# Performance work log

Measured on AMD Instinct MI355X. Metric: run time of the kernel, lower is better.

Reference implementation:

```python
import jax, jax.numpy as jnp
import numpy as np


def setup_inputs() -> dict:
    key = jax.random.key(0)
    ks = jax.random.split(key, 8)
    B, N, C = 4, 2048, 1024
    H, hd, lr, R = 16, 64, 20, 200  # R = low_rank * rank_multi
    s = lambda k, shape, fan: jax.random.normal(k, shape, jnp.float32) / np.sqrt(fan)
    return {
        'x': jax.random.normal(ks[0], (B, N, C), jnp.float32),
        'qk_w': s(ks[1], (2 * C, C), C),
        'proj_w': s(ks[2], (C, C), C),
        'proj_b': jnp.zeros((C,), jnp.float32),
        'we': s(ks[3], (H, R, lr), R),
        'wr': s(ks[4], (H, R, lr), R),
        'cw_w': s(ks[5], (hd, 2 * lr), 2 * lr),
        'cw_b': jnp.zeros((hd,), jnp.float32),
    }


def _l2norm(v, eps=1e-12):
    # matches F.normalize(p=2, dim=-1): x / max(||x||, eps)
    n = jnp.sqrt(jnp.sum(v * v, axis=-1, keepdims=True))
    return v / jnp.maximum(n, eps)


def reference(x, qk_w, proj_w, proj_b, we, wr, cw_w, cw_b):
    B, N, C = x.shape
    H, R, lr = we.shape  # heads, subsample len, low_rank
    hd = C // H
    # qk projection -> q,k: [B,H,N,hd]
    qk = (x @ qk_w.T).reshape(B, N, 2, H, hd).transpose(2, 0, 3, 1, 4)
    q, k = qk[0], qk[1]
    # gen_weights: subsample N positions (embed_len > low_rank*rank_multi branch)
    idx = np.linspace(0, N - 1, R).astype(np.int64)  # static, trunc like torch
    xh = x.transpose(0, 2, 1).reshape(B, H, hd, N)[:, :, :, idx]  # [B,H,hd,R]
    we_b = jnp.einsum('bhdr,hre->bhde', xh, we)  # [B,H,hd,lr]
    wr_b = jnp.einsum('bhdr,hre->bhde', xh, wr)
    # feature map + low-rank scores
    q = _l2norm(q)
    k = _l2norm(k)
    escore = jnp.einsum('bhnd,bhde->bhne', q, we_b)  # [B,H,N,lr]
    rscore = jnp.einsum('bhnd,bhde->bhne', k, wr_b)
    score = jnp.concatenate([escore, rscore], axis=-1)  # [B,H,N,2lr]
    attn = score @ cw_w.T + cw_b  # [B,H,N,hd]
    attn = attn.transpose(0, 2, 1, 3).reshape(B, N, C)
    out = attn @ proj_w.T + proj_b  # dropout is identity at eval
    return out
```

## Files before the change

### kernel.cpp

```cpp
#include <hip/hip_runtime.h>
#include <hip/hip_bf16.h>

constexpr int B_  = 4;
constexpr int N_  = 2048;
constexpr int C_  = 1024;
constexpr int H_  = 16;
constexpr int HD  = 64;
constexpr int LR  = 20;
constexpr int RS  = 200;
constexpr int RP  = 224;
constexpr int RPAD = 232;

typedef __attribute__((ext_vector_type(8))) short bf16x8;
typedef __attribute__((ext_vector_type(4))) float f32x4;

__device__ __forceinline__ float b2f_raw(unsigned short u) {
    union { unsigned int i; float f; } v;
    v.i = ((unsigned int)u) << 16;
    return v.f;
}
__device__ __forceinline__ unsigned short f2b(float f) {
    __hip_bfloat16 h = __float2bfloat16(f);
    return *(unsigned short*)&h;
}
template <bool BF>
__device__ __forceinline__ float ldg(const void* p, size_t i) {
    if constexpr (BF) return b2f_raw(((const unsigned short*)p)[i]);
    else              return ((const float*)p)[i];
}

__device__ __forceinline__ void async_load16(const unsigned short* g, unsigned short* l) {
    __builtin_amdgcn_global_load_lds(
        (const __attribute__((address_space(1))) unsigned int*)(const void*)g,
        (__attribute__((address_space(3))) unsigned int*)(void*)l,
        16, 0, 0);
}

__device__ __forceinline__ bool detect_bf16(const unsigned int* __restrict__ x) {
    const int lane = threadIdx.x & 63;
    int cnt = 0;
    #pragma unroll
    for (int i = 0; i < 16; ++i) {
        const unsigned int w = x[lane * 16 + i];
        const unsigned int e = (w >> 7) & 0xFFu;
        cnt += (e >= 103u && e <= 140u) ? 1 : 0;
    }
    #pragma unroll
    for (int s = 1; s < 64; s <<= 1) cnt += __shfl_xor(cnt, s, 64);
    return cnt > 512;
}

struct CvtArgs {
    const void* src[5];
    unsigned short* dst[5];
    int size[5];
};

template <bool BF>
__device__ void gwc_body(const void* __restrict__ x_raw,
                         const void* __restrict__ we_raw,
                         const void* __restrict__ wr_raw,
                         const void* __restrict__ cw_raw,
                         unsigned short* __restrict__ we2t,
                         unsigned short* __restrict__ wr2t,
                         unsigned short* __restrict__ sx,
                         unsigned short* __restrict__ sx2,
                         unsigned short* __restrict__ wl,
                         float* __restrict__ cwl,
                         int blk) {
    const int bh    = blk >> 2;
    const int dhalf = (blk >> 1) & 1;
    const int qk    = blk & 1;
    const int b = bh >> 4;
    const int h = bh & 15;
    const int t    = threadIdx.x;
    const int wave = t >> 6;
    const int lane = t & 63;

    {
        const int dout = t >> 2;
        const int e0   = (t & 3) * 5;
        #pragma unroll
        for (int i = 0; i < 5; ++i)
            cwl[dout * LR + e0 + i] =
                ldg<BF>(cw_raw, (size_t)dout * 2 * LR + qk * LR + e0 + i);
    }

    const int dlo = lane & 31;
    const int rhi = lane >> 5;
    for (int rd = wave; rd < 100; rd += 4) {
        const int r  = rd * 2 + rhi;
        const int ir = (r * (N_ - 1)) / (RS - 1);
        const size_t idx = ((size_t)b * N_ + ir) * C_ + h * HD + dhalf * 32 + dlo;
        unsigned short v;
        if constexpr (BF) v = ((const unsigned short*)x_raw)[idx];
        else              v = f2b(((const float*)x_raw)[idx]);
        sx[r * 32 + (dlo ^ (r & 31))] = v;
    }
    __syncthreads();

    if (t < RP) {
        const int r = t;
        float w20[LR];
        if (r < RS) {
            const void* wsrc = qk ? wr_raw : we_raw;
            #pragma unroll
            for (int e = 0; e < LR; ++e)
                w20[e] = ldg<BF>(wsrc, ((size_t)h * RS + r) * LR + e);
        } else {
            #pragma unroll
            for (int e = 0; e < LR; ++e) w20[e] = 0.f;
        }
        for (int dout = 0; dout < HD; ++dout) {
            float s = 0.f;
            #pragma unroll
            for (int e = 0; e < LR; ++e) s += w20[e] * cwl[dout * LR + e];
            wl[dout * RPAD + r] = f2b(s);
        }
    }

    for (int o = t; o < 32 * RP; o += 256) {
        const int din = o / RP;
        const int r   = o % RP;
        const unsigned short v = (r < RS) ? sx[r * 32 + (din ^ (r & 31))]
                                          : (unsigned short)0;
        sx2[din * RPAD + r] = v;
    }
    __syncthreads();

    const int lq = lane >> 4;
    const int lm = lane & 15;
    f32x4 acc[2];
    acc[0] = 0.f; acc[1] = 0.f;
    for (int ks = 0; ks < RP / 32; ++ks) {
        bf16x8 av = *(const bf16x8*)&wl[(wave * 16 + lm) * RPAD + ks * 32 + lq * 8];
        #pragma unroll
        for (int j = 0; j < 2; ++j) {
            bf16x8 bv = *(const bf16x8*)&sx2[(j * 16 + lm) * RPAD + ks * 32 + lq * 8];
            acc[j] = __builtin_amdgcn_mfma_f32_16x16x32_bf16(av, bv, acc[j], 0, 0, 0);
        }
    }
    unsigned short* dst = (qk ? wr2t : we2t) + (size_t)bh * HD * HD;
    #pragma unroll
    for (int j = 0; j < 2; ++j)
        #pragma unroll
        for (int r = 0; r < 4; ++r) {
            const int dout = wave * 16 + lq * 4 + r;
            const int din  = dhalf * 32 + j * 16 + lm;
            dst[dout * HD + din] = f2b(acc[j][r]);
        }
}

__global__ __launch_bounds__(256)
void fused_prep_kernel(CvtArgs args,
                       const void* __restrict__ we_raw,
                       const void* __restrict__ wr_raw,
                       const void* __restrict__ cw_raw,
                       unsigned short* __restrict__ we2t,
                       unsigned short* __restrict__ wr2t) {
    __shared__ __align__(16) unsigned short sx[RP * 32];
    __shared__ __align__(16) unsigned short sx2[32 * RPAD];
    __shared__ __align__(16) unsigned short wl[64 * RPAD];
    __shared__ float cwl[64 * LR];
    const bool isbf = detect_bf16((const unsigned int*)args.src[0]);
    const int y = blockIdx.y;
    if (y == 0) {
        if (isbf) return;
        const int n4 = args.size[0] >> 2;
        const int stride = 2048 * 256;
        for (int i = blockIdx.x * 256 + threadIdx.x; i < n4; i += stride) {
            const float4 v = ((const float4*)args.src[0])[i];
            ushort4 o;
            o.x = f2b(v.x); o.y = f2b(v.y); o.z = f2b(v.z); o.w = f2b(v.w);
            ((ushort4*)args.dst[0])[i] = o;
        }
    } else if (y == 1) {
        if (isbf) return;
        const int n1 = args.size[1] >> 2;
        const int n2 = args.size[2] >> 2;
        const int n3 = args.size[3] >> 2;
        const int n4 = args.size[4] >> 2;
        const int tot = n1 + n2 + n3 + n4;
        const int stride = 2048 * 256;
        for (int i = blockIdx.x * 256 + threadIdx.x; i < tot; i += stride) {
            const float4* s; ushort4* d; int j;
            if (i < n1)                { s = (const float4*)args.src[1]; d = (ushort4*)args.dst[1]; j = i; }
            else if (i < n1 + n2)      { s = (const float4*)args.src[2]; d = (ushort4*)args.dst[2]; j = i - n1; }
            else if (i < n1 + n2 + n3) { s = (const float4*)args.src[3]; d = (ushort4*)args.dst[3]; j = i - n1 - n2; }
            else                       { s = (const float4*)args.src[4]; d = (ushort4*)args.dst[4]; j = i - n1 - n2 - n3; }
            const float4 v = s[j];
            ushort4 o;
            o.x = f2b(v.x); o.y = f2b(v.y); o.z = f2b(v.z); o.w = f2b(v.w);
            d[j] = o;
        }
    } else {
        const int blk = blockIdx.x;
        if (blk >= 256) return;
        if (isbf) gwc_body<true>(args.src[0], we_raw, wr_raw, cw_raw,
                                 we2t, wr2t, sx, sx2, wl, cwl, blk);
        else      gwc_body<false>(args.src[0], we_raw, wr_raw, cw_raw,
                                  we2t, wr2t, sx, sx2, wl, cwl, blk);
    }
}

__global__ __launch_bounds__(256, 2)
void gemm1_score_kernel(const void* __restrict__ x_raw,
                        const void* __restrict__ qkw_raw,
                        const void* __restrict__ cwb_raw,
                        const unsigned short* __restrict__ xb,
                        const unsigned short* __restrict__ qkwb,
                        const unsigned short* __restrict__ cwbb,
                        const unsigned short* __restrict__ we2t,
                        const unsigned short* __restrict__ wr2t,
                        unsigned short* __restrict__ attn) {
    constexpr int QS = 72;
    __shared__ __align__(16) unsigned short pool[32768];
    unsigned short* const AsBase = pool;
    unsigned short* const BsBase = pool + 16384;
    unsigned short* qn = pool;
    unsigned short* kn = pool + 128 * QS;

    const bool isbf = detect_bf16((const unsigned int*)x_raw);
    const unsigned short* xs  = isbf ? (const unsigned short*)x_raw   : xb;
    const unsigned short* qks = isbf ? (const unsigned short*)qkw_raw : qkwb;
    const unsigned short* cwb = isbf ? (const unsigned short*)cwb_raw : cwbb;

    const int t    = threadIdx.x;
    const int wave = t >> 6;
    const int lane = t & 63;
    const int lin     = blockIdx.y * 16 + blockIdx.x;
    const int logical = (lin & 7) * 128 + (lin >> 3);
    const int h       = logical & 15;
    const int mt      = logical >> 4;
    const int m0      = mt * 128;
    const int K       = C_;

    const int srow  = lane >> 3;
    const int sunit = (lane & 7) ^ srow;
    const unsigned short* gA = xs + (size_t)(m0 + wave * 32 + srow) * K + sunit * 8;
    const int vb = wave * 32;
    const size_t brow = (vb < 64) ? (size_t)(h * HD + vb)
                                  : (size_t)(C_ + h * HD + (vb - 64));
    const unsigned short* gB = qks + (brow + srow) * K + sunit * 8;

    const int wr = (wave >> 1) * 64;
    const int wc = (wave & 1) * 64;
    const int lq = lane >> 4;
    const int lm = lane & 15;
    const int c0 = (lq ^ (lm & 7)) * 8;

    f32x4 acc[4][4];
    #pragma unroll
    for (int i = 0; i < 4; ++i)
        #pragma unroll
        for (int j = 0; j < 4; ++j) acc[i][j] = 0.f;

    auto stage = [&](int buf) {
        unsigned short* dA = AsBase + buf * 8192 + wave * 2048;
        unsigned short* dB = BsBase + buf * 8192 + wave * 2048;
        #pragma unroll
        for (int i = 0; i < 4; ++i) {
            async_load16(gA + (size_t)i * 8 * K, dA + i * 512);
            async_load16(gB + (size_t)i * 8 * K, dB + i * 512);
        }
        gA += 64; gB += 64;
    };
    auto compute = [&](int buf) {
        const unsigned short* As = AsBase + buf * 8192;
        const unsigned short* Bs = BsBase + buf * 8192;
        #pragma unroll
        for (int ks = 0; ks < 2; ++ks) {
            const int cc = c0 ^ (ks * 32);
            bf16x8 af[4], bfr[4];
            #pragma unroll
            for (int i = 0; i < 4; ++i)
                af[i] = *(const bf16x8*)&As[(wr + i * 16 + lm) * 64 + cc];
            #pragma unroll
            for (int j = 0; j < 4; ++j)
                bfr[j] = *(const bf16x8*)&Bs[(wc + j * 16 + lm) * 64 + cc];
            #pragma unroll
            for (int i = 0; i < 4; ++i)
                #pragma unroll
                for (int j = 0; j < 4; ++j)
                    acc[i][j] = __builtin_amdgcn_mfma_f32_16x16x32_bf16(
                        af[i], bfr[j], acc[i][j], 0, 0, 0);
        }
    };

    constexpr int NTK = C_ / 64;
    stage(0);
    __syncthreads();
    for (int kt = 0; kt < NTK - 1; ++kt) {
        stage((kt + 1) & 1);
        compute(kt & 1);
        __syncthreads();
    }
    compute((NTK - 1) & 1);
    __syncthreads();

    unsigned short* dst = (wc == 0) ? qn : kn;
    #pragma unroll
    for (int i = 0; i < 4; ++i) {
        float inv[4];
        #pragma unroll
        for (int r = 0; r < 4; ++r) {
            float s = 0.f;
            #pragma unroll
            for (int j = 0; j < 4; ++j) s += acc[i][j][r] * acc[i][j][r];
            s += __shfl_xor(s, 1, 64);
            s += __shfl_xor(s, 2, 64);
            s += __shfl_xor(s, 4, 64);
            s += __shfl_xor(s, 8, 64);
            inv[r] = 1.f / fmaxf(sqrtf(s), 1e-12f);
        }
        #pragma unroll
        for (int j = 0; j < 4; ++j)
            #pragma unroll
            for (int r = 0; r < 4; ++r) {
                const int row = wr + i * 16 + lq * 4 + r;
                dst[row * QS + j * 16 + lm] = f2b(acc[i][j][r] * inv[r]);
            }
    }
    __syncthreads();

    const int b  = mt >> 4;
    const int bh = b * H_ + h;
    const unsigned short* wq = we2t + (size_t)bh * HD * HD;
    const unsigned short* wk = wr2t + (size_t)bh * HD * HD;

    bf16x8 bq[2][4], bk[2][4];
    #pragma unroll
    for (int t2 = 0; t2 < 2; ++t2)
        #pragma unroll
        for (int j = 0; j < 4; ++j) {
            const int dout = j * 16 + lm;
            bq[t2][j] = *(const bf16x8*)&wq[dout * HD + t2 * 32 + lq * 8];
            bk[t2][j] = *(const bf16x8*)&wk[dout * HD + t2 * 32 + lq * 8];
        }

    f32x4 accS[2][4];
    #pragma unroll
    for (int rt = 0; rt < 2; ++rt)
        #pragma unroll
        for (int j = 0; j < 4; ++j) accS[rt][j] = 0.f;

    #pragma unroll
    for (int rt = 0; rt < 2; ++rt) {
        const int lr = wave * 32 + rt * 16 + lm;
        bf16x8 aq0 = *(const bf16x8*)&qn[lr * QS + lq * 8];
        bf16x8 aq1 = *(const bf16x8*)&qn[lr * QS + 32 + lq * 8];
        bf16x8 ak0 = *(const bf16x8*)&kn[lr * QS + lq * 8];
        bf16x8 ak1 = *(const bf16x8*)&kn[lr * QS + 32 + lq * 8];
        #pragma unroll
        for (int j = 0; j < 4; ++j) {
            accS[rt][j] = __builtin_amdgcn_mfma_f32_16x16x32_bf16(aq0, bq[0][j], accS[rt][j], 0, 0, 0);
            accS[rt][j] = __builtin_amdgcn_mfma_f32_16x16x32_bf16(aq1, bq[1][j], accS[rt][j], 0, 0, 0);
            accS[rt][j] = __builtin_amdgcn_mfma_f32_16x16x32_bf16(ak0, bk[0][j], accS[rt][j], 0, 0, 0);
            accS[rt][j] = __builtin_amdgcn_mfma_f32_16x16x32_bf16(ak1, bk[1][j], accS[rt][j], 0, 0, 0);
        }
    }

    #pragma unroll
    for (int rt = 0; rt < 2; ++rt)
        #pragma unroll
        for (int j = 0; j < 4; ++j) {
            const int dout = j * 16 + lm;
            const float bv = b2f_raw(cwb[dout]);
            #pragma unroll
            for (int r = 0; r < 4; ++r) {
                const int row = m0 + wave * 32 + rt * 16 + lq * 4 + r;
                attn[(size_t)row * C_ + h * HD + dout] = f2b(accS[rt][j][r] + bv);
            }
        }
}

template <bool OBF>
__device__ void mfma_gemm_body64(const unsigned short* __restrict__ A,
                                 const unsigned short* __restrict__ W,
                                 const unsigned short* __restrict__ bias,
                                 void* __restrict__ out,
                                 int M, int N, int K, int m0, int n0) {
    __shared__ __align__(16) unsigned short AsBase[16384];
    __shared__ __align__(16) unsigned short BsBase[16384];

    const int t    = threadIdx.x;
    const int wave = t >> 6;
    const int lane = t & 63;

    const int srow  = lane >> 3;
    const int sunit = (lane & 7) ^ srow;
    const unsigned short* gA = A + (size_t)(m0 + wave * 32 + srow) * K + sunit * 8;
    const unsigned short* gB = W + (size_t)(n0 + wave * 32 + srow) * K + sunit * 8;

    const int wr = (wave >> 1) * 64;
    const int wc = (wave & 1) * 64;
    const int lq = lane >> 4;
    const int lm = lane & 15;
    const int c0 = (lq ^ (lm & 7)) * 8;

    f32x4 acc[4][4];
    #pragma unroll
    for (int i = 0; i < 4; ++i)
        #pragma unroll
        for (int j = 0; j < 4; ++j) acc[i][j] = 0.f;

    auto stage = [&](int buf) {
        unsigned short* dA = AsBase + buf * 8192 + wave * 2048;
        unsigned short* dB = BsBase + buf * 8192 + wave * 2048;
        #pragma unroll
        for (int i = 0; i < 4; ++i) {
            async_load16(gA + (size_t)i * 8 * K, dA + i * 512);
            async_load16(gB + (size_t)i * 8 * K, dB + i * 512);
        }
        gA += 64; gB += 64;
    };
    auto compute = [&](int buf) {
        const unsigned short* As = AsBase + buf * 8192;
        const unsigned short* Bs = BsBase + buf * 8192;
        #pragma unroll
        for (int ks = 0; ks < 2; ++ks) {
            const int cc = c0 ^ (ks * 32);
            bf16x8 af[4], bfr[4];
            #pragma unroll
            for (int i = 0; i < 4; ++i)
                af[i] = *(const bf16x8*)&As[(wr + i * 16 + lm) * 64 + cc];
            #pragma unroll
            for (int j = 0; j < 4; ++j)
                bfr[j] = *(const bf16x8*)&Bs[(wc + j * 16 + lm) * 64 + cc];
            #pragma unroll
            for (int i = 0; i < 4; ++i)
                #pragma unroll
                for (int j = 0; j < 4; ++j)
                    acc[i][j] = __builtin_amdgcn_mfma_f32_16x16x32_bf16(
                        af[i], bfr[j], acc[i][j], 0, 0, 0);
        }
    };

    const int NTK = K / 64;
    stage(0);
    __syncthreads();
    for (int kt = 0; kt < NTK - 1; ++kt) {
        stage((kt + 1) & 1);
        compute(kt & 1);
        __syncthreads();
    }
    compute((NTK - 1) & 1);

    #pragma unroll
    for (int i = 0; i < 4; ++i) {
        #pragma unroll
        for (int j = 0; j < 4; ++j) {
            const int col = n0 + wc + j * 16 + lm;
            const float bv = b2f_raw(bias[col]);
            #pragma unroll
            for (int r = 0; r < 4; ++r) {
                const int row = m0 + wr + i * 16 + lq * 4 + r;
                const float v = acc[i][j][r] + bv;
                if constexpr (OBF)
                    ((__hip_bfloat16*)out)[(size_t)row * N + col] = __float2bfloat16(v);
                else
                    ((float*)out)[(size_t)row * N + col] = v;
            }
        }
    }
}

__global__ __launch_bounds__(256, 2)
void gemm2_kernel(const void* __restrict__ x_raw,
                  const void* __restrict__ pw_raw,
                  const void* __restrict__ pb_raw,
                  const unsigned short* __restrict__ attn,
                  const unsigned short* __restrict__ pwb,
                  const unsigned short* __restrict__ pbb,
                  void* __restrict__ out) {
    const bool isbf = detect_bf16((const unsigned int*)x_raw);
    const unsigned short* W = isbf ? (const unsigned short*)pw_raw : pwb;
    const unsigned short* bias = isbf ? (const unsigned short*)pb_raw : pbb;
    const int lin     = blockIdx.y * 8 + blockIdx.x;
    const int logical = (lin & 7) * 64 + (lin >> 3);
    const int n0      = (logical & 7) * 128;
    const int m0      = (logical >> 3) * 128;
    if (isbf) mfma_gemm_body64<true>(attn, W, bias, out, B_ * N_, C_, C_, m0, n0);
    else      mfma_gemm_body64<false>(attn, W, bias, out, B_ * N_, C_, C_, m0, n0);
}

extern "C" void kernel_launch(void* const* d_in, const int* in_sizes, int n_in,
                              void* d_out, int out_size, void* d_ws, size_t ws_size,
                              hipStream_t stream) {
    (void)in_sizes; (void)n_in; (void)out_size; (void)ws_size;

    char* ws = (char*)d_ws;
    size_t off = 0;
    auto alloc = [&](size_t bytes) {
        char* p = ws + off;
        off += (bytes + 255) & ~(size_t)255;
        return p;
    };

    unsigned short* xb    = (unsigned short*)alloc((size_t)B_ * N_ * C_ * 2);
    unsigned short* qkwb  = (unsigned short*)alloc((size_t)2 * C_ * C_ * 2);
    unsigned short* pwb   = (unsigned short*)alloc((size_t)C_ * C_ * 2);
    unsigned short* pbb   = (unsigned short*)alloc((size_t)C_ * 2);
    unsigned short* cwbb  = (unsigned short*)alloc((size_t)HD * 2);
    unsigned short* attn  = (unsigned short*)alloc((size_t)B_ * N_ * C_ * 2);
    unsigned short* we2t  = (unsigned short*)alloc((size_t)B_ * H_ * HD * HD * 2);
    unsigned short* wr2t  = (unsigned short*)alloc((size_t)B_ * H_ * HD * HD * 2);

    const int M = B_ * N_;

    CvtArgs ca;
    ca.src[0] = d_in[0]; ca.dst[0] = xb;   ca.size[0] = B_ * N_ * C_;
    ca.src[1] = d_in[1]; ca.dst[1] = qkwb; ca.size[1] = 2 * C_ * C_;
    ca.src[2] = d_in[2]; ca.dst[2] = pwb;  ca.size[2] = C_ * C_;
    ca.src[3] = d_in[3]; ca.dst[3] = pbb;  ca.size[3] = C_;
    ca.src[4] = d_in[7]; ca.dst[4] = cwbb; ca.size[4] = HD;
    fused_prep_kernel<<<dim3(2048, 3), 256, 0, stream>>>(
        ca, d_in[4], d_in[5], d_in[6], we2t, wr2t);

    gemm1_score_kernel<<<dim3(16, M / 128), 256, 0, stream>>>(
        d_in[0], d_in[1], d_in[7], xb, qkwb, cwbb, we2t, wr2t, attn);

    gemm2_kernel<<<dim3(C_ / 128, M / 128), 256, 0, stream>>>(
        d_in[0], d_in[2], d_in[3], attn, pwb, pbb, d_out);
}
```

Baseline: 214.5 us.

## Enlarge GEMM tiles to 256 rows with 512 threads and triple-buffered async loads

Both the QK-projection/score kernel and the output-projection GEMM now use 512-thread blocks that each cover 256 rows, and the LDS pool holds three stages. The old double buffer with a full __syncthreads per step is replaced by a three-stage ring. Inline s_waitcnt vmcnt(6) plus a barrier lets the next two tiles' global-to-LDS loads stay in flight during compute. The aim is better latency hiding and more reuse of each weight tile. In exchange, LDS per block grows to about 144 KB, occupancy drops to one block per CU, and the grid halves, which may leave some CUs idle.

Result: faster. 190.9 us (-11.0%).

```diff
diff --git a/kernel.cpp b/kernel.cpp
--- a/kernel.cpp
+++ b/kernel.cpp
@@ -13,6 +13,9 @@
 
 typedef __attribute__((ext_vector_type(8))) short bf16x8;
 typedef __attribute__((ext_vector_type(4))) float f32x4;
+
+#define WAITBAR6 asm volatile("s_waitcnt vmcnt(6) lgkmcnt(0)\n\ts_barrier" ::: "memory")
+#define WAITBAR0 asm volatile("s_waitcnt vmcnt(0) lgkmcnt(0)\n\ts_barrier" ::: "memory")
 
 __device__ __forceinline__ float b2f_raw(unsigned short u) {
     union { unsigned int i; float f; } v;
@@ -203,7 +206,7 @@
     }
 }
 
-__global__ __launch_bounds__(256, 2)
+__global__ __launch_bounds__(512, 1)
 void gemm1_score_kernel(const void* __restrict__ x_raw,
                         const void* __restrict__ qkw_raw,
                         const void* __restrict__ cwb_raw,
@@ -214,11 +217,9 @@
                         const unsigned short* __restrict__ wr2t,
                         unsigned short* __restrict__ attn) {
     constexpr int QS = 72;
-    __shared__ __align__(16) unsigned short pool[32768];
-    unsigned short* const AsBase = pool;
-    unsigned short* const BsBase = pool + 16384;
+    __shared__ __align__(16) unsigned short pool[73728];
     unsigned short* qn = pool;
-    unsigned short* kn = pool + 128 * QS;
+    unsigned short* kn = pool + 256 * QS;
 
     const bool isbf = detect_bf16((const unsigned int*)x_raw);
     const unsigned short* xs  = isbf ? (const unsigned short*)x_raw   : xb;
@@ -229,22 +230,22 @@
     const int wave = t >> 6;
     const int lane = t & 63;
     const int lin     = blockIdx.y * 16 + blockIdx.x;
-    const int logical = (lin & 7) * 128 + (lin >> 3);
+    const int logical = (lin & 7) * 64 + (lin >> 3);
     const int h       = logical & 15;
     const int mt      = logical >> 4;
-    const int m0      = mt * 128;
+    const int m0      = mt * 256;
     const int K       = C_;
 
     const int srow  = lane >> 3;
     const int sunit = (lane & 7) ^ srow;
     const unsigned short* gA = xs + (size_t)(m0 + wave * 32 + srow) * K + sunit * 8;
-    const int vb = wave * 32;
-    const size_t brow = (vb < 64) ? (size_t)(h * HD + vb)
-                                  : (size_t)(C_ + h * HD + (vb - 64));
-    const unsigned short* gB = qks + (brow + srow) * K + sunit * 8;
+    const int vb0 = wave * 16 + srow;
+    const size_t brow = (vb0 < 64) ? (size_t)(h * HD + vb0)
+                                   : (size_t)(C_ + h * HD + (vb0 - 64));
+    const unsigned short* gB = qks + brow * K + sunit * 8;
 
     const int wr = (wave >> 1) * 64;
-    const int wc = (wave & 1) * 64;
+    const int wn = wave & 1;
     const int lq = lane >> 4;
     const int lm = lane & 15;
     const int c0 = (lq ^ (lm & 7)) * 8;
@@ -255,19 +256,20 @@
         #pragma unroll
         for (int j = 0; j < 4; ++j) acc[i][j] = 0.f;
 
-    auto stage = [&](int buf) {
-        unsigned short* dA = AsBase + buf * 8192 + wave * 2048;
-        unsigned short* dB = BsBase + buf * 8192 + wave * 2048;
-        #pragma unroll
-        for (int i = 0; i < 4; ++i) {
+    auto stage = [&](int b) {
+        unsigned short* dA = pool + b * 24576 + wave * 2048;
+        unsigned short* dB = pool + b * 24576 + 16384 + wave * 1024;
+        #pragma unroll
+        for (int i = 0; i < 4; ++i)
             async_load16(gA + (size_t)i * 8 * K, dA + i * 512);
+        #pragma unroll
+        for (int i = 0; i < 2; ++i)
             async_load16(gB + (size_t)i * 8 * K, dB + i * 512);
-        }
         gA += 64; gB += 64;
     };
-    auto compute = [&](int buf) {
-        const unsigned short* As = AsBase + buf * 8192;
-        const unsigned short* Bs = BsBase + buf * 8192;
+    auto compute = [&](int b) {
+        const unsigned short* As = pool + b * 24576;
+        const unsigned short* Bs = As + 16384;
         #pragma unroll
         for (int ks = 0; ks < 2; ++ks) {
             const int cc = c0 ^ (ks * 32);
@@ -277,7 +279,7 @@
                 af[i] = *(const bf16x8*)&As[(wr + i * 16 + lm) * 64 + cc];
             #pragma unroll
             for (int j = 0; j < 4; ++j)
-                bfr[j] = *(const bf16x8*)&Bs[(wc + j * 16 + lm) * 64 + cc];
+                bfr[j] = *(const bf16x8*)&Bs[(wn * 64 + j * 16 + lm) * 64 + cc];
             #pragma unroll
             for (int i = 0; i < 4; ++i)
                 #pragma unroll
@@ -287,18 +289,17 @@
         }
     };
 
-    constexpr int NTK = C_ / 64;
-    stage(0);
+    constexpr int NT = C_ / 64;
+    stage(0); stage(1);
+    for (int kt = 0; kt < NT; ++kt) {
+        if (kt + 2 < NT)      { WAITBAR6; stage((kt + 2) % 3); }
+        else if (kt + 1 < NT) { WAITBAR6; }
+        else                  { WAITBAR0; }
+        compute(kt % 3);
+    }
     __syncthreads();
-    for (int kt = 0; kt < NTK - 1; ++kt) {
-        stage((kt + 1) & 1);
-        compute(kt & 1);
-        __syncthreads();
-    }
-    compute((NTK - 1) & 1);
-    __syncthreads();
-
-    unsigned short* dst = (wc == 0) ? qn : kn;
+
+    unsigned short* dst = (wn == 0) ? qn : kn;
     #pragma unroll
     for (int i = 0; i < 4; ++i) {
         float inv[4];
@@ -323,7 +324,7 @@
     }
     __syncthreads();
 
-    const int b  = mt >> 4;
+    const int b  = mt >> 3;
     const int bh = b * H_ + h;
     const unsigned short* wq = we2t + (size_t)bh * HD * HD;
     const unsigned short* wk = wr2t + (size_t)bh * HD * HD;
@@ -375,14 +376,12 @@
 }
 
 template <bool OBF>
-__device__ void mfma_gemm_body64(const unsigned short* __restrict__ A,
-                                 const unsigned short* __restrict__ W,
-                                 const unsigned short* __restrict__ bias,
-                                 void* __restrict__ out,
-                                 int M, int N, int K, int m0, int n0) {
-    __shared__ __align__(16) unsigned short AsBase[16384];
-    __shared__ __align__(16) unsigned short BsBase[16384];
-
+__device__ void mfma_gemm_body3buf(const unsigned short* __restrict__ A,
+                                   const unsigned short* __restrict__ W,
+                                   const unsigned short* __restrict__ bias,
+                                   void* __restrict__ out,
+                                   int N, int K, int m0, int n0,
+                                   unsigned short* pool) {
     const int t    = threadIdx.x;
     const int wave = t >> 6;
     const int lane = t & 63;
@@ -390,10 +389,10 @@
     const int srow  = lane >> 3;
     const int sunit = (lane & 7) ^ srow;
     const unsigned short* gA = A + (size_t)(m0 + wave * 32 + srow) * K + sunit * 8;
-    const unsigned short* gB = W + (size_t)(n0 + wave * 32 + srow) * K + sunit * 8;
+    const unsigned short* gB = W + (size_t)(n0 + wave * 16 + srow) * K + sunit * 8;
 
     const int wr = (wave >> 1) * 64;
-    const int wc = (wave & 1) * 64;
+    const int wn = wave & 1;
     const int lq = lane >> 4;
     const int lm = lane & 15;
     const int c0 = (lq ^ (lm & 7)) * 8;
@@ -404,19 +403,20 @@
         #pragma unroll
         for (int j = 0; j < 4; ++j) acc[i][j] = 0.f;
 
-    auto stage = [&](int buf) {
-        unsigned short* dA = AsBase + buf * 8192 + wave * 2048;
-        unsigned short* dB = BsBase + buf * 8192 + wave * 2048;
-        #pragma unroll
-        for (int i = 0; i < 4; ++i) {
+    auto stage = [&](int b) {
+        unsigned short* dA = pool + b * 24576 + wave * 2048;
+        unsigned short* dB = pool + b * 24576 + 16384 + wave * 1024;
+        #pragma unroll
+        for (int i = 0; i < 4; ++i)
             async_load16(gA + (size_t)i * 8 * K, dA + i * 512);
+        #pragma unroll
+        for (int i = 0; i < 2; ++i)
             async_load16(gB + (size_t)i * 8 * K, dB + i * 512);
-        }
         gA += 64; gB += 64;
     };
-    auto compute = [&](int buf) {
-        const unsigned short* As = AsBase + buf * 8192;
-        const unsigned short* Bs = BsBase + buf * 8192;
+    auto compute = [&](int b) {
+        const unsigned short* As = pool + b * 24576;
+        const unsigned short* Bs = As + 16384;
         #pragma unroll
         for (int ks = 0; ks < 2; ++ks) {
             const int cc = c0 ^ (ks * 32);
@@ -426,7 +426,7 @@
                 af[i] = *(const bf16x8*)&As[(wr + i * 16 + lm) * 64 + cc];
             #pragma unroll
             for (int j = 0; j < 4; ++j)
-                bfr[j] = *(const bf16x8*)&Bs[(wc + j * 16 + lm) * 64 + cc];
+                bfr[j] = *(const bf16x8*)&Bs[(wn * 64 + j * 16 + lm) * 64 + cc];
             #pragma unroll
             for (int i = 0; i < 4; ++i)
                 #pragma unroll
@@ -436,21 +436,20 @@
         }
     };
 
-    const int NTK = K / 64;
-    stage(0);
-    __syncthreads();
-    for (int kt = 0; kt < NTK - 1; ++kt) {
-        stage((kt + 1) & 1);
-        compute(kt & 1);
-        __syncthreads();
-    }
-    compute((NTK - 1) & 1);
+    const int NT = K / 64;
+    stage(0); stage(1);
+    for (int kt = 0; kt < NT; ++kt) {
+        if (kt + 2 < NT)      { WAITBAR6; stage((kt + 2) % 3); }
+        else if (kt + 1 < NT) { WAITBAR6; }
+        else                  { WAITBAR0; }
+        compute(kt % 3);
+    }
 
     #pragma unroll
     for (int i = 0; i < 4; ++i) {
         #pragma unroll
         for (int j = 0; j < 4; ++j) {
-            const int col = n0 + wc + j * 16 + lm;
+            const int col = n0 + wn * 64 + j * 16 + lm;
             const float bv = b2f_raw(bias[col]);
             #pragma unroll
             for (int r = 0; r < 4; ++r) {
@@ -465,7 +464,7 @@
     }
 }
 
-__global__ __launch_bounds__(256, 2)
+__global__ __launch_bounds__(512, 1)
 void gemm2_kernel(const void* __restrict__ x_raw,
                   const void* __restrict__ pw_raw,
                   const void* __restrict__ pb_raw,
@@ -473,15 +472,16 @@
                   const unsigned short* __restrict__ pwb,
                   const unsigned short* __restrict__ pbb,
                   void* __restrict__ out) {
+    __shared__ __align__(16) unsigned short pool[73728];
     const bool isbf = detect_bf16((const unsigned int*)x_raw);
     const unsigned short* W = isbf ? (const unsigned short*)pw_raw : pwb;
     const unsigned short* bias = isbf ? (const unsigned short*)pb_raw : pbb;
     const int lin     = blockIdx.y * 8 + blockIdx.x;
-    const int logical = (lin & 7) * 64 + (lin >> 3);
+    const int logical = (lin & 7) * 32 + (lin >> 3);
     const int n0      = (logical & 7) * 128;
-    const int m0      = (logical >> 3) * 128;
-    if (isbf) mfma_gemm_body64<true>(attn, W, bias, out, B_ * N_, C_, C_, m0, n0);
-    else      mfma_gemm_body64<false>(attn, W, bias, out, B_ * N_, C_, C_, m0, n0);
+    const int m0      = (logical >> 3) * 256;
+    if (isbf) mfma_gemm_body3buf<true>(attn, W, bias, out, C_, C_, m0, n0, pool);
+    else      mfma_gemm_body3buf<false>(attn, W, bias, out, C_, C_, m0, n0, pool);
 }
 
 extern "C" void kernel_launch(void* const* d_in, const int* in_sizes, int n_in,
@@ -506,8 +506,6 @@
     unsigned short* we2t  = (unsigned short*)alloc((size_t)B_ * H_ * HD * HD * 2);
     unsigned short* wr2t  = (unsigned short*)alloc((size_t)B_ * H_ * HD * HD * 2);
 
-    const int M = B_ * N_;
-
     CvtArgs ca;
     ca.src[0] = d_in[0]; ca.dst[0] = xb;   ca.size[0] = B_ * N_ * C_;
     ca.src[1] = d_in[1]; ca.dst[1] = qkwb; ca.size[1] = 2 * C_ * C_;
@@ -517,9 +515,9 @@
     fused_prep_kernel<<<dim3(2048, 3), 256, 0, stream>>>(
         ca, d_in[4], d_in[5], d_in[6], we2t, wr2t);
 
-    gemm1_score_kernel<<<dim3(16, M / 128), 256, 0, stream>>>(
+    gemm1_score_kernel<<<dim3(16, 32), 512, 0, stream>>>(
         d_in[0], d_in[1], d_in[7], xb, qkwb, cwbb, we2t, wr2t, attn);
 
-    gemm2_kernel<<<dim3(C_ / 128, M / 128), 256, 0, stream>>>(
+    gemm2_kernel<<<dim3(8, 32), 512, 0, stream>>>(
         d_in[0], d_in[2], d_in[3], attn, pwb, pbb, d_out);
 }
```

## Triple-buffer gemm2 with 256x128 tiles and 512-thread blocks

Applied to the files above, without the earlier changes.

Reworks the output projection GEMM to use 512-thread blocks that compute 256x128 tiles, so each B tile is shared across eight waves. The K loop moves from double to triple buffering with explicit vmcnt waits and barriers, keeping two stages of loads in flight. The aim is better operand reuse and more overlap of global loads with MFMA work. The cost is one block per CU with 144KB of LDS, fewer blocks in the grid (256), and hand-written waitcnt assembly that depends on the exact count of outstanding loads.

Result: faster. 190.4 us (-11.2%).

```diff
diff --git a/kernel.cpp b/kernel.cpp
--- a/kernel.cpp
+++ b/kernel.cpp
@@ -13,6 +13,9 @@
 
 typedef __attribute__((ext_vector_type(8))) short bf16x8;
 typedef __attribute__((ext_vector_type(4))) float f32x4;
+
+#define WAITBAR6 asm volatile("s_waitcnt vmcnt(6) lgkmcnt(0)\n\ts_barrier" ::: "memory")
+#define WAITBAR0 asm volatile("s_waitcnt vmcnt(0) lgkmcnt(0)\n\ts_barrier" ::: "memory")
 
 __device__ __forceinline__ float b2f_raw(unsigned short u) {
     union { unsigned int i; float f; } v;
@@ -375,14 +378,12 @@
 }
 
 template <bool OBF>
-__device__ void mfma_gemm_body64(const unsigned short* __restrict__ A,
-                                 const unsigned short* __restrict__ W,
-                                 const unsigned short* __restrict__ bias,
-                                 void* __restrict__ out,
-                                 int M, int N, int K, int m0, int n0) {
-    __shared__ __align__(16) unsigned short AsBase[16384];
-    __shared__ __align__(16) unsigned short BsBase[16384];
-
+__device__ void mfma_gemm_body3buf(const unsigned short* __restrict__ A,
+                                   const unsigned short* __restrict__ W,
+                                   const unsigned short* __restrict__ bias,
+                                   void* __restrict__ out,
+                                   int N, int K, int m0, int n0,
+                                   unsigned short* pool) {
     const int t    = threadIdx.x;
     const int wave = t >> 6;
     const int lane = t & 63;
@@ -390,10 +391,10 @@
     const int srow  = lane >> 3;
     const int sunit = (lane & 7) ^ srow;
     const unsigned short* gA = A + (size_t)(m0 + wave * 32 + srow) * K + sunit * 8;
-    const unsigned short* gB = W + (size_t)(n0 + wave * 32 + srow) * K + sunit * 8;
+    const unsigned short* gB = W + (size_t)(n0 + wave * 16 + srow) * K + sunit * 8;
 
     const int wr = (wave >> 1) * 64;
-    const int wc = (wave & 1) * 64;
+    const int wn = wave & 1;
     const int lq = lane >> 4;
     const int lm = lane & 15;
     const int c0 = (lq ^ (lm & 7)) * 8;
@@ -404,19 +405,20 @@
         #pragma unroll
         for (int j = 0; j < 4; ++j) acc[i][j] = 0.f;
 
-    auto stage = [&](int buf) {
-        unsigned short* dA = AsBase + buf * 8192 + wave * 2048;
-        unsigned short* dB = BsBase + buf * 8192 + wave * 2048;
-        #pragma unroll
-        for (int i = 0; i < 4; ++i) {
+    auto stage = [&](int b) {
+        unsigned short* dA = pool + b * 24576 + wave * 2048;
+        unsigned short* dB = pool + b * 24576 + 16384 + wave * 1024;
+        #pragma unroll
+        for (int i = 0; i < 4; ++i)
             async_load16(gA + (size_t)i * 8 * K, dA + i * 512);
+        #pragma unroll
+        for (int i = 0; i < 2; ++i)
             async_load16(gB + (size_t)i * 8 * K, dB + i * 512);
-        }
         gA += 64; gB += 64;
     };
-    auto compute = [&](int buf) {
-        const unsigned short* As = AsBase + buf * 8192;
-        const unsigned short* Bs = BsBase + buf * 8192;
+    auto compute = [&](int b) {
+        const unsigned short* As = pool + b * 24576;
+        const unsigned short* Bs = As + 16384;
         #pragma unroll
         for (int ks = 0; ks < 2; ++ks) {
             const int cc = c0 ^ (ks * 32);
@@ -426,7 +428,7 @@
                 af[i] = *(const bf16x8*)&As[(wr + i * 16 + lm) * 64 + cc];
             #pragma unroll
             for (int j = 0; j < 4; ++j)
-                bfr[j] = *(const bf16x8*)&Bs[(wc + j * 16 + lm) * 64 + cc];
+                bfr[j] = *(const bf16x8*)&Bs[(wn * 64 + j * 16 + lm) * 64 + cc];
             #pragma unroll
             for (int i = 0; i < 4; ++i)
                 #pragma unroll
@@ -436,21 +438,20 @@
         }
     };
 
-    const int NTK = K / 64;
-    stage(0);
-    __syncthreads();
-    for (int kt = 0; kt < NTK - 1; ++kt) {
-        stage((kt + 1) & 1);
-        compute(kt & 1);
-        __syncthreads();
-    }
-    compute((NTK - 1) & 1);
+    const int NT = K / 64;
+    stage(0); stage(1);
+    for (int kt = 0; kt < NT; ++kt) {
+        if (kt + 2 < NT)      { WAITBAR6; stage((kt + 2) % 3); }
+        else if (kt + 1 < NT) { WAITBAR6; }
+        else                  { WAITBAR0; }
+        compute(kt % 3);
+    }
 
     #pragma unroll
     for (int i = 0; i < 4; ++i) {
         #pragma unroll
         for (int j = 0; j < 4; ++j) {
-            const int col = n0 + wc + j * 16 + lm;
+            const int col = n0 + wn * 64 + j * 16 + lm;
             const float bv = b2f_raw(bias[col]);
             #pragma unroll
             for (int r = 0; r < 4; ++r) {
@@ -465,7 +466,7 @@
     }
 }
 
-__global__ __launch_bounds__(256, 2)
+__global__ __launch_bounds__(512, 1)
 void gemm2_kernel(const void* __restrict__ x_raw,
                   const void* __restrict__ pw_raw,
                   const void* __restrict__ pb_raw,
@@ -473,15 +474,16 @@
                   const unsigned short* __restrict__ pwb,
                   const unsigned short* __restrict__ pbb,
                   void* __restrict__ out) {
+    __shared__ __align__(16) unsigned short pool[73728];
     const bool isbf = detect_bf16((const unsigned int*)x_raw);
     const unsigned short* W = isbf ? (const unsigned short*)pw_raw : pwb;
     const unsigned short* bias = isbf ? (const unsigned short*)pb_raw : pbb;
     const int lin     = blockIdx.y * 8 + blockIdx.x;
-    const int logical = (lin & 7) * 64 + (lin >> 3);
+    const int logical = (lin & 7) * 32 + (lin >> 3);
     const int n0      = (logical & 7) * 128;
-    const int m0      = (logical >> 3) * 128;
-    if (isbf) mfma_gemm_body64<true>(attn, W, bias, out, B_ * N_, C_, C_, m0, n0);
-    else      mfma_gemm_body64<false>(attn, W, bias, out, B_ * N_, C_, C_, m0, n0);
+    const int m0      = (logical >> 3) * 256;
+    if (isbf) mfma_gemm_body3buf<true>(attn, W, bias, out, C_, C_, m0, n0, pool);
+    else      mfma_gemm_body3buf<false>(attn, W, bias, out, C_, C_, m0, n0, pool);
 }
 
 extern "C" void kernel_launch(void* const* d_in, const int* in_sizes, int n_in,
@@ -520,6 +522,6 @@
     gemm1_score_kernel<<<dim3(16, M / 128), 256, 0, stream>>>(
         d_in[0], d_in[1], d_in[7], xb, qkwb, cwbb, we2t, wr2t, attn);
 
-    gemm2_kernel<<<dim3(C_ / 128, M / 128), 256, 0, stream>>>(
+    gemm2_kernel<<<dim3(8, 32), 512, 0, stream>>>(
         d_in[0], d_in[2], d_in[3], attn, pwb, pbb, d_out);
 }
```
